# Kernel optimization log

Hardware: AMD Instinct MI355X
Metric: run time of the kernel (lower is better)

## Reference

```python
import jax, jax.numpy as jnp
import numpy as np
from math import log2

N_QUBITS = 11
N_LAYERS = 2
DEGREE = 3
N_TIMESTEPS = 8
BSZ = 64
DIM = 2 ** N_QUBITS
N_ROTS = 4 * N_QUBITS * N_LAYERS  # 88


def _ry(theta):
    # batched RY(theta): (B,) -> (B,2,2) complex64
    h = 0.5 * theta
    c, s = jnp.cos(h), jnp.sin(h)
    U = jnp.stack([jnp.stack([c, -s], -1), jnp.stack([s, c], -1)], -2)
    return U.astype(jnp.complex64)


def _rx(theta):
    # batched RX(theta): (B,) -> (B,2,2) complex64
    h = 0.5 * theta
    c = jnp.cos(h).astype(jnp.complex64)
    s = (-1j) * jnp.sin(h).astype(jnp.complex64)
    return jnp.stack([jnp.stack([c, s], -1), jnp.stack([s, c], -1)], -2)


def _apply_1q(state, U, w):
    # state: (B,) + (2,)*n ; apply per-batch 2x2 U on wire w
    s = jnp.moveaxis(state, w + 1, 1)
    shp = s.shape
    s = s.reshape(shp[0], 2, -1)
    s = jnp.einsum('bij,bjr->bir', U, s)
    return jnp.moveaxis(s.reshape(shp), 1, w + 1)


def _apply_crx(state, theta, c_w, t_w):
    # controlled-RX: apply RX on target wire t_w where control wire c_w is |1>
    U = _rx(theta)
    s = jnp.moveaxis(state, (c_w + 1, t_w + 1), (1, 2))
    shp = s.shape
    s = s.reshape(shp[0], 2, 2, -1)
    s1 = jnp.einsum('bij,bjr->bir', U, s[:, 1])
    s = jnp.concatenate([s[:, :1], s1[:, None]], axis=1).reshape(shp)
    return jnp.moveaxis(s, (1, 2), (c_w + 1, t_w + 1))


def _sim14_evolve(state, params):
    # faithful sim14_circuit (v3 fixed RY-CRX gate set), batched angles
    n = state.ndim - 1
    layers = params.shape[1] // (4 * n)
    idx = 0
    for _ in range(layers):
        for i in range(n):
            state = _apply_1q(state, _ry(params[:, idx]), i); idx += 1
        for i in range(n - 1, -1, -1):
            state = _apply_crx(state, params[:, idx], i, (i + 1) % n); idx += 1
        for i in range(n):
            state = _apply_1q(state, _ry(params[:, idx]), i); idx += 1
        for i in [n - 1] + list(range(n - 1)):
            state = _apply_crx(state, params[:, idx], i, (i - 1) % n); idx += 1
    return state


def _apply_unitaries(base, uparams, coeffs):
    # apply_unitaries_pl: repeat_interleave + evolve + LCU einsum
    bsz, T, n_rots = uparams.shape
    dim = base.shape[1]
    n = int(round(log2(dim)))
    flat = uparams.reshape(bsz * T, n_rots)
    rep = jnp.repeat(base, T, axis=0).reshape((bsz * T,) + (2,) * n)
    ev = _sim14_evolve(rep, flat).reshape(bsz, T, dim)
    return jnp.einsum('bti,bt->bi', ev, coeffs.astype(jnp.complex64))


def setup_inputs() -> dict:
    key = jax.random.key(0)
    k1, k2, k3, k4 = jax.random.split(key, 4)
    base_states = jax.random.normal(k1, (BSZ, DIM), dtype=jnp.float32)
    unitary_params = jax.random.normal(k2, (BSZ, N_TIMESTEPS, N_ROTS), dtype=jnp.float32)
    lcu_coeffs = jax.random.normal(k3, (BSZ, N_TIMESTEPS), dtype=jnp.float32)
    poly_coeffs = jax.random.normal(k4, (DEGREE + 1,), dtype=jnp.float32)
    return {"base_states": base_states, "unitary_params": unitary_params,
            "lcu_coeffs": lcu_coeffs, "poly_coeffs": poly_coeffs}


def reference(base_states, unitary_params, lcu_coeffs, poly_coeffs):
    # evaluate_polynomial_state_pl (QSVT polynomial state preparation)
    base = base_states.astype(jnp.complex64)
    base = base / jnp.linalg.norm(base, axis=1, keepdims=True)  # valid quantum state
    pc = poly_coeffs.astype(jnp.complex64)
    acc = pc[0] * base
    working = base
    for k in range(1, poly_coeffs.shape[0]):
        working = _apply_unitaries(working, unitary_params, lcu_coeffs)
        acc = acc + pc[k] * working
    out = acc / jnp.sum(jnp.abs(poly_coeffs)).astype(jnp.complex64)
    # return real/imag stacked so output is real-valued: (bsz, dim, 2)
    return jnp.stack([out.real, out.imag], axis=-1)
```

## Files before the change

kernel.cpp:

```cpp
#include <hip/hip_runtime.h>
#include <utility>

#define DIM 2048
#define NQ 11
#define NROT 88
#define BSZ 64
#define NT 8
#define NPC 4

#if __has_builtin(__builtin_amdgcn_permlane16_swap)
#define HAVE_PL16 1
#else
#define HAVE_PL16 0
#endif
#if __has_builtin(__builtin_amdgcn_permlane32_swap)
#define HAVE_PL32 1
#else
#define HAVE_PL32 0
#endif

constexpr int g_type(int G) {
    int j = G % 44;
    return (j < 11 || (j >= 22 && j < 33)) ? 0 : 1;
}
constexpr int g_pt(int G) {
    int j = G % 44;
    if (j < 11) return 10 - j;
    if (j < 22) { int i = 21 - j; int tw = (i + 1 == NQ) ? 0 : i + 1; return 10 - tw; }
    if (j < 33) return 10 - (j - 22);
    if (j == 33) return 1;
    int i = j - 34; int tw = (i + 10) % NQ; return 10 - tw;
}
constexpr int g_pcb(int G) {
    int j = G % 44;
    if (j >= 11 && j < 22) { int i = 21 - j; return 10 - i; }
    if (j == 33) return 0;
    if (j >= 34) { int i = j - 34; return 10 - i; }
    return -1;
}
constexpr int block_parity(int G) {
    int c = 0;
    for (int g = 0; g < G; ++g) if (g_pt(g) >= 8) c ^= 1;
    return c;
}
constexpr bool use_sum_tier(int lb) {
    return (lb == 4 && HAVE_PL16) || (lb == 5 && HAVE_PL32);
}

template<int G>
__device__ __forceinline__ void get_cs(float c0, float s0, float c1, float s1,
                                       float& c, float& s) {
    if constexpr (G < 64) {
        c = __int_as_float(__builtin_amdgcn_readlane(__float_as_int(c0), G));
        s = __int_as_float(__builtin_amdgcn_readlane(__float_as_int(s0), G));
    } else {
        c = __int_as_float(__builtin_amdgcn_readlane(__float_as_int(c1), G - 64));
        s = __int_as_float(__builtin_amdgcn_readlane(__float_as_int(s1), G - 64));
    }
}

template<int LB>
__device__ __forceinline__ float lxp(float x) {
    if constexpr (LB == 0) {
        return __int_as_float(__builtin_amdgcn_update_dpp(
            __float_as_int(x), __float_as_int(x), 0xB1, 0xF, 0xF, true));
    } else if constexpr (LB == 1) {
        return __int_as_float(__builtin_amdgcn_update_dpp(
            __float_as_int(x), __float_as_int(x), 0x4E, 0xF, 0xF, true));
    } else if constexpr (LB == 2) {
        return __int_as_float(__builtin_amdgcn_ds_swizzle(__float_as_int(x), 0x101F));
    } else if constexpr (LB == 3) {
        return __int_as_float(__builtin_amdgcn_update_dpp(
            __float_as_int(x), __float_as_int(x), 0x128, 0xF, 0xF, true));
    } else if constexpr (LB == 4) {
        return __int_as_float(__builtin_amdgcn_ds_swizzle(__float_as_int(x), 0x401F));
    } else {
        return __shfl_xor(x, 32, 64);
    }
}

template<int LB>
__device__ __forceinline__ float lxsum(float x) {
#if HAVE_PL16
    if constexpr (LB == 4) {
        unsigned u = __float_as_uint(x);
        auto r = __builtin_amdgcn_permlane16_swap(u, u, false, false);
        return __uint_as_float(r[0]) + __uint_as_float(r[1]);
    }
#endif
#if HAVE_PL32
    if constexpr (LB == 5) {
        unsigned u = __float_as_uint(x);
        auto r = __builtin_amdgcn_permlane32_swap(u, u, false, false);
        return __uint_as_float(r[0]) + __uint_as_float(r[1]);
    }
#endif
    return x + lxp<LB>(x);
}

template<int G>
__device__ __forceinline__ void apply_gate(
    float2 (&R)[2], float2 (&I)[2],
    float c0, float s0, float c1, float s1,
    float4* __restrict__ exbuf, const int tid)
{
    constexpr int type = g_type(G);
    constexpr int pt   = g_pt(G);
    constexpr int pcb  = g_pcb(G);
    float c, s;
    get_cs<G>(c0, s0, c1, s1, c, s);

    if constexpr (pt == 0) {
        if constexpr (type == 0) {
#pragma unroll
            for (int m = 0; m < 2; ++m) {
                float er = R[m].x, orr = R[m].y, ei = I[m].x, oi = I[m].y;
                R[m].x = c*er - s*orr;  R[m].y = s*er + c*orr;
                I[m].x = c*ei - s*oi;   I[m].y = s*ei + c*oi;
            }
        } else if constexpr (pcb == 1) {
            float er = R[1].x, orr = R[1].y, ei = I[1].x, oi = I[1].y;
            R[1].x = c*er + s*oi;   I[1].x = c*ei - s*orr;
            R[1].y = c*orr + s*ei;  I[1].y = c*oi - s*er;
        } else {
            const bool ctrl = (tid >> (pcb - 2)) & 1;
            if (ctrl) {
#pragma unroll
                for (int m = 0; m < 2; ++m) {
                    float er = R[m].x, orr = R[m].y, ei = I[m].x, oi = I[m].y;
                    R[m].x = c*er + s*oi;   I[m].x = c*ei - s*orr;
                    R[m].y = c*orr + s*ei;  I[m].y = c*oi - s*er;
                }
            }
        }
    } else if constexpr (pt == 1) {
        if constexpr (type == 0) {
            float2 l = R[0], h = R[1], li = I[0], hi = I[1];
            R[0].x = c*l.x - s*h.x;   R[0].y = c*l.y - s*h.y;
            R[1].x = s*l.x + c*h.x;   R[1].y = s*l.y + c*h.y;
            I[0].x = c*li.x - s*hi.x; I[0].y = c*li.y - s*hi.y;
            I[1].x = s*li.x + c*hi.x; I[1].y = s*li.y + c*hi.y;
        } else if constexpr (pcb == 0) {
            float lr = R[0].y, li = I[0].y, hr = R[1].y, hi = I[1].y;
            R[0].y = c*lr + s*hi;   I[0].y = c*li - s*hr;
            R[1].y = c*hr + s*li;   I[1].y = c*hi - s*lr;
        } else {
            const bool ctrl = (tid >> (pcb - 2)) & 1;
            if (ctrl) {
                float2 l = R[0], h = R[1], li = I[0], hi = I[1];
                R[0].x = c*l.x + s*hi.x;  R[0].y = c*l.y + s*hi.y;
                I[0].x = c*li.x - s*h.x;  I[0].y = c*li.y - s*h.y;
                R[1].x = c*h.x + s*li.x;  R[1].y = c*h.y + s*li.y;
                I[1].x = c*hi.x - s*l.x;  I[1].y = c*hi.y - s*l.y;
            }
        }
    } else if constexpr (pt <= 7) {
        constexpr int lb = pt - 2;
        if constexpr (use_sum_tier(lb)) {
            if constexpr (type == 0) {
                const float sg = ((tid >> lb) & 1) ? s : -s;
                const float k1 = c - sg;
#pragma unroll
                for (int m = 0; m < 2; ++m) {
                    float srx = lxsum<lb>(R[m].x), sry = lxsum<lb>(R[m].y);
                    float six = lxsum<lb>(I[m].x), siy = lxsum<lb>(I[m].y);
                    R[m].x = k1*R[m].x + sg*srx;  R[m].y = k1*R[m].y + sg*sry;
                    I[m].x = k1*I[m].x + sg*six;  I[m].y = k1*I[m].y + sg*siy;
                }
            } else if constexpr (pcb == 0) {
#pragma unroll
                for (int m = 0; m < 2; ++m) {
                    float sR = lxsum<lb>(R[m].y), sI = lxsum<lb>(I[m].y);
                    float r = R[m].y, i = I[m].y;
                    R[m].y = c*r - s*i + s*sI;
                    I[m].y = c*i + s*r - s*sR;
                }
            } else if constexpr (pcb == 1) {
                float sRx = lxsum<lb>(R[1].x), sRy = lxsum<lb>(R[1].y);
                float sIx = lxsum<lb>(I[1].x), sIy = lxsum<lb>(I[1].y);
                float rx = R[1].x, ry = R[1].y, ix = I[1].x, iy = I[1].y;
                R[1].x = c*rx - s*ix + s*sIx;  R[1].y = c*ry - s*iy + s*sIy;
                I[1].x = c*ix + s*rx - s*sRx;  I[1].y = c*iy + s*ry - s*sRy;
            } else {
                const bool ctrl = (tid >> (pcb - 2)) & 1;
                if (ctrl) {
#pragma unroll
                    for (int m = 0; m < 2; ++m) {
                        float sRx = lxsum<lb>(R[m].x), sRy = lxsum<lb>(R[m].y);
                        float sIx = lxsum<lb>(I[m].x), sIy = lxsum<lb>(I[m].y);
                        float rx = R[m].x, ry = R[m].y, ix = I[m].x, iy = I[m].y;
                        R[m].x = c*rx - s*ix + s*sIx;  R[m].y = c*ry - s*iy + s*sIy;
                        I[m].x = c*ix + s*rx - s*sRx;  I[m].y = c*iy + s*ry - s*sRy;
                    }
                }
            }
        } else {
            if constexpr (type == 0) {
                const float sg = ((tid >> lb) & 1) ? s : -s;
#pragma unroll
                for (int m = 0; m < 2; ++m) {
                    float prx = lxp<lb>(R[m].x), pry = lxp<lb>(R[m].y);
                    float pix = lxp<lb>(I[m].x), piy = lxp<lb>(I[m].y);
                    R[m].x = c*R[m].x + sg*prx;  R[m].y = c*R[m].y + sg*pry;
                    I[m].x = c*I[m].x + sg*pix;  I[m].y = c*I[m].y + sg*piy;
                }
            } else if constexpr (pcb == 0) {
#pragma unroll
                for (int m = 0; m < 2; ++m) {
                    float pry = lxp<lb>(R[m].y), piy = lxp<lb>(I[m].y);
                    R[m].y = c*R[m].y + s*piy;
                    I[m].y = c*I[m].y - s*pry;
                }
            } else if constexpr (pcb == 1) {
                float prx = lxp<lb>(R[1].x), pry = lxp<lb>(R[1].y);
                float pix = lxp<lb>(I[1].x), piy = lxp<lb>(I[1].y);
                R[1].x = c*R[1].x + s*pix;  R[1].y = c*R[1].y + s*piy;
                I[1].x = c*I[1].x - s*prx;  I[1].y = c*I[1].y - s*pry;
            } else {
                const bool ctrl = (tid >> (pcb - 2)) & 1;
                if (ctrl) {
#pragma unroll
                    for (int m = 0; m < 2; ++m) {
                        float prx = lxp<lb>(R[m].x), pry = lxp<lb>(R[m].y);
                        float pix = lxp<lb>(I[m].x), piy = lxp<lb>(I[m].y);
                        R[m].x = c*R[m].x + s*pix;  R[m].y = c*R[m].y + s*piy;
                        I[m].x = c*I[m].x - s*prx;  I[m].y = c*I[m].y - s*pry;
                    }
                }
            }
        }
    } else {
        constexpr int par = block_parity(G);
        float4* buf = exbuf + par * 1024;
        const int ptid = tid ^ (1 << (pt - 2));
        if constexpr (type == 0) {
#pragma unroll
            for (int m = 0; m < 2; ++m)
                buf[m * 512 + tid] = make_float4(R[m].x, R[m].y, I[m].x, I[m].y);
            __syncthreads();
            const float sg = ((tid >> (pt - 2)) & 1) ? s : -s;
#pragma unroll
            for (int m = 0; m < 2; ++m) {
                float4 v = buf[m * 512 + ptid];
                R[m].x = c*R[m].x + sg*v.x;  R[m].y = c*R[m].y + sg*v.y;
                I[m].x = c*I[m].x + sg*v.z;  I[m].y = c*I[m].y + sg*v.w;
            }
        } else if constexpr (pcb == 0) {
            float2* f2 = (float2*)buf;
#pragma unroll
            for (int m = 0; m < 2; ++m)
                f2[m * 512 + tid] = make_float2(R[m].y, I[m].y);
            __syncthreads();
#pragma unroll
            for (int m = 0; m < 2; ++m) {
                float2 v = f2[m * 512 + ptid];
                R[m].y = c*R[m].y + s*v.y;
                I[m].y = c*I[m].y - s*v.x;
            }
        } else if constexpr (pcb == 1) {
            buf[tid] = make_float4(R[1].x, R[1].y, I[1].x, I[1].y);
            __syncthreads();
            float4 v = buf[ptid];
            R[1].x = c*R[1].x + s*v.z;  R[1].y = c*R[1].y + s*v.w;
            I[1].x = c*I[1].x - s*v.x;  I[1].y = c*I[1].y - s*v.y;
        } else {
            const bool ctrl = (tid >> (pcb - 2)) & 1;
            if (ctrl) {
#pragma unroll
                for (int m = 0; m < 2; ++m)
                    buf[m * 512 + tid] = make_float4(R[m].x, R[m].y, I[m].x, I[m].y);
            }
            __syncthreads();
            if (ctrl) {
#pragma unroll
                for (int m = 0; m < 2; ++m) {
                    float4 v = buf[m * 512 + ptid];
                    R[m].x = c*R[m].x + s*v.z;  R[m].y = c*R[m].y + s*v.w;
                    I[m].x = c*I[m].x - s*v.x;  I[m].y = c*I[m].y - s*v.y;
                }
            }
        }
    }
}

template<int... Gs>
__device__ __forceinline__ void apply_all(std::integer_sequence<int, Gs...>,
    float2 (&R)[2], float2 (&I)[2],
    float c0, float s0, float c1, float s1,
    float4* __restrict__ exbuf, const int tid)
{
    (apply_gate<Gs>(R, I, c0, s0, c1, s1, exbuf, tid), ...);
}

template<int MODE>
__global__ __launch_bounds__(512, 4) void evolve_kernel(
    const void* __restrict__ src, const float* __restrict__ uparams,
    const float* __restrict__ lcu, float2* __restrict__ pout,
    const float* __restrict__ pcoef, float2* __restrict__ acc, int kprev)
{
    __shared__ float4 exbuf[2048];
    __shared__ float red[9];

    const int b = blockIdx.x >> 3;
    const int t = blockIdx.x & 7;
    const int tid = threadIdx.x;
    const int lane = tid & 63;

    const float* __restrict__ th_row = uparams + (size_t)(b * NT + t) * NROT;
    float th0 = 0.5f * th_row[lane];
    float th1 = (lane < NROT - 64) ? 0.5f * th_row[64 + lane] : 0.f;
    float tc0 = cosf(th0), ts0 = sinf(th0);
    float tc1 = cosf(th1), ts1 = sinf(th1);

    float2 R[2], I[2];
    if constexpr (MODE == 0) {
        const float4* b4 = (const float4*)((const float*)src + (size_t)b * DIM);
        float4 v = b4[tid];
        float loc = v.x*v.x + v.y*v.y + v.z*v.z + v.w*v.w;
        for (int off = 32; off > 0; off >>= 1) loc += __shfl_down(loc, off, 64);
        if ((tid & 63) == 0) red[tid >> 6] = loc;
        __syncthreads();
        if (tid == 0) { float sm = 0.f; for (int w = 0; w < 8; ++w) sm += red[w]; red[8] = sm; }
        __syncthreads();
        const float inv = rsqrtf(red[8]);
        R[0] = make_float2(v.x * inv, v.y * inv);
        R[1] = make_float2(v.z * inv, v.w * inv);
        I[0] = make_float2(0.f, 0.f);
        I[1] = make_float2(0.f, 0.f);
        if (t == 0) {
            const float p0 = pcoef[0];
            float4* a4 = (float4*)(acc + (size_t)b * DIM);
            a4[tid*2+0] = make_float4(p0*R[0].x, 0.f, p0*R[0].y, 0.f);
            a4[tid*2+1] = make_float4(p0*R[1].x, 0.f, p0*R[1].y, 0.f);
        }
    } else if constexpr (MODE == 1) {
        R[0] = R[1] = I[0] = I[1] = make_float2(0.f, 0.f);
        const float2* s2 = (const float2*)src;
        for (int cc = 0; cc < NT; ++cc) {
            const float4* p4 = (const float4*)(s2 + ((size_t)b * NT + cc) * DIM);
#pragma unroll
            for (int m = 0; m < 2; ++m) {
                float4 v = p4[tid*2+m];
                R[m].x += v.x; I[m].x += v.y; R[m].y += v.z; I[m].y += v.w;
            }
        }
        if (t == 0) {
            const float pk = pcoef[kprev];
            float4* a4 = (float4*)(acc + (size_t)b * DIM);
#pragma unroll
            for (int m = 0; m < 2; ++m) {
                float4 v = a4[tid*2+m];
                v.x += pk * R[m].x; v.y += pk * I[m].x;
                v.z += pk * R[m].y; v.w += pk * I[m].y;
                a4[tid*2+m] = v;
            }
        }
    } else {
        const float2* s2 = (const float2*)src;
        const float4* p4 = (const float4*)(s2 + (size_t)b * DIM);
#pragma unroll
        for (int m = 0; m < 2; ++m) {
            float4 v = p4[tid*2+m];
            R[m].x = v.x; I[m].x = v.y; R[m].y = v.z; I[m].y = v.w;
        }
    }

    apply_all(std::make_integer_sequence<int, NROT>{}, R, I,
              tc0, ts0, tc1, ts1, exbuf, tid);

    const float coeff = lcu[b * NT + t];
    float4* o4 = (float4*)(pout + ((size_t)b * NT + t) * DIM);
#pragma unroll
    for (int m = 0; m < 2; ++m)
        o4[tid*2+m] = make_float4(coeff*R[m].x, coeff*I[m].x, coeff*R[m].y, coeff*I[m].y);
}

__global__ __launch_bounds__(256) void final_kernel(
    const float2* __restrict__ partial, const float* __restrict__ pcoef,
    const float2* __restrict__ acc, float* __restrict__ out)
{
    int b = blockIdx.x >> 3;
    int i = ((blockIdx.x & 7) << 8) | threadIdx.x;
    float sr = 0.f, si = 0.f;
    for (int c = 0; c < NT; ++c) {
        float2 v = partial[((size_t)b * NT + c) * DIM + i];
        sr += v.x; si += v.y;
    }
    float sabs = 0.f;
    for (int q = 0; q < NPC; ++q) sabs += fabsf(pcoef[q]);
    float invn = 1.0f / sabs;
    float pk = pcoef[NPC - 1];
    float2 a = acc[(size_t)b * DIM + i];
    out[((size_t)b * DIM + i) * 2 + 0] = (a.x + pk * sr) * invn;
    out[((size_t)b * DIM + i) * 2 + 1] = (a.y + pk * si) * invn;
}

__global__ __launch_bounds__(256) void setup_kernel(
    const float* __restrict__ base, const float* __restrict__ pc,
    float2* __restrict__ working, float2* __restrict__ acc)
{
    int b = blockIdx.x;
    int tid = threadIdx.x;
    __shared__ float red[4];
    float ssum = 0.f;
    for (int i = tid; i < DIM; i += 256) {
        float v = base[b * DIM + i];
        ssum += v * v;
    }
    for (int off = 32; off > 0; off >>= 1) ssum += __shfl_down(ssum, off, 64);
    if ((tid & 63) == 0) red[tid >> 6] = ssum;
    __syncthreads();
    if (tid == 0) red[0] = red[0] + red[1] + red[2] + red[3];
    __syncthreads();
    float inv = rsqrtf(red[0]);
    float p0 = pc[0];
    for (int i = tid; i < DIM; i += 256) {
        float v = base[b * DIM + i] * inv;
        working[b * DIM + i] = make_float2(v, 0.f);
        acc[b * DIM + i] = make_float2(p0 * v, 0.f);
    }
}

__global__ __launch_bounds__(256) void reduce_kernel(
    const float2* __restrict__ partial, const float* __restrict__ pcoef,
    float2* __restrict__ working, float2* __restrict__ acc,
    float* __restrict__ out, int k, int last)
{
    int b = blockIdx.x >> 3;
    int i = ((blockIdx.x & 7) << 8) | threadIdx.x;
    float pk = pcoef[k];
    float sr = 0.f, si = 0.f;
    for (int c = 0; c < NT; ++c) {
        float2 v = partial[((size_t)b * NT + c) * DIM + i];
        sr += v.x; si += v.y;
    }
    working[b * DIM + i] = make_float2(sr, si);
    float2 a = acc[b * DIM + i];
    a.x += pk * sr; a.y += pk * si;
    acc[b * DIM + i] = a;
    if (last) {
        float sabs = 0.f;
        for (int q = 0; q < NPC; ++q) sabs += fabsf(pcoef[q]);
        float invn = 1.0f / sabs;
        out[((size_t)b * DIM + i) * 2 + 0] = a.x * invn;
        out[((size_t)b * DIM + i) * 2 + 1] = a.y * invn;
    }
}

extern "C" void kernel_launch(void* const* d_in, const int* in_sizes, int n_in,
                              void* d_out, int out_size, void* d_ws, size_t ws_size,
                              hipStream_t stream) {
    const float* base = (const float*)d_in[0];
    const float* upar = (const float*)d_in[1];
    const float* lcu  = (const float*)d_in[2];
    const float* pc   = (const float*)d_in[3];
    float* out = (float*)d_out;

    const size_t plane = (size_t)BSZ * DIM * sizeof(float2);
    char* ws = (char*)d_ws;

    if (ws_size >= (1 + 3 * (size_t)NT) * plane) {
        float2* acc = (float2*)ws;
        float2* pA  = (float2*)(ws + plane);
        float2* pB  = (float2*)(ws + plane + (size_t)NT * plane);
        float2* pC  = (float2*)(ws + plane + (size_t)2 * NT * plane);
        evolve_kernel<0><<<BSZ * NT, 512, 0, stream>>>(base, upar, lcu, pA, pc, acc, 0);
        evolve_kernel<1><<<BSZ * NT, 512, 0, stream>>>(pA,   upar, lcu, pB, pc, acc, 1);
        evolve_kernel<1><<<BSZ * NT, 512, 0, stream>>>(pB,   upar, lcu, pC, pc, acc, 2);
        final_kernel<<<BSZ * 8, 256, 0, stream>>>(pC, pc, acc, out);
    } else {
        float2* working = (float2*)ws;
        float2* acc     = (float2*)(ws + plane);
        float2* pA      = (float2*)(ws + 2 * plane);
        setup_kernel<<<BSZ, 256, 0, stream>>>(base, pc, working, acc);
        for (int k = 1; k <= NPC - 1; ++k) {
            evolve_kernel<2><<<BSZ * NT, 512, 0, stream>>>(working, upar, lcu, pA, pc, acc, 0);
            reduce_kernel<<<BSZ * 8, 256, 0, stream>>>(pA, pc, working, acc, out,
                                                       k, (k == NPC - 1) ? 1 : 0);
        }
    }
}
```

Before: 90.09 us.

## Replace per-gate LDS exchanges with qubit-permuting transposes between gate groups

Gates on high qubits (bits 8-10, which span thread-block positions) previously each needed their own shared-memory exchange and barrier. The gate sequence is now reordered into 96 ops, with four swizzled shared-memory transposes that swap qubit bits (2,3,5)<->(8,9,10). This lets most gates run in registers or via intra-wave lane permutes. It cuts the number of block-wide barriers and LDS round trips, at the cost of full-state transposes and more complex gate bookkeeping.

New measurement: 85.24 us. 5.4% less time.

```diff
diff --git a/kernel.cpp b/kernel.cpp
--- a/kernel.cpp
+++ b/kernel.cpp
@@ -38,14 +38,37 @@
     if (j >= 34) { int i = j - 34; return 10 - i; }
     return -1;
 }
-constexpr int block_parity(int G) {
-    int c = 0;
-    for (int g = 0; g < G; ++g) if (g_pt(g) >= 8) c ^= 1;
-    return c;
-}
 constexpr bool use_sum_tier(int lb) {
     return (lb == 4 && HAVE_PL16) || (lb == 5 && HAVE_PL32);
 }
+
+constexpr int tmap(int b) {
+    if (b == 2) return 8;  if (b == 8) return 2;
+    if (b == 3) return 9;  if (b == 9) return 3;
+    if (b == 5) return 10; if (b == 10) return 5;
+    return b;
+}
+
+constexpr int lop_j(int k) {
+    if (k < 8)  return 3 + k;
+    if (k == 8) return -1;
+    if (k < 12) return k - 9;
+    if (k == 12) return 11;
+    if (k == 13) return -1;
+    if (k < 22) return 12 + (k - 14);
+    if (k == 22) return -1;
+    if (k == 23) return 20;
+    if (k == 24) return 21;
+    if (k < 31) { int w[6] = {0, 1, 2, 3, 9, 10}; return 22 + w[k - 25]; }
+    if (k < 36) return 33 + (k - 31);
+    if (k == 36) return -1;
+    if (k < 42) return 26 + (k - 37);
+    return 38 + (k - 42);
+}
+constexpr bool lop_B(int k) {
+    return (k >= 9 && k <= 12) || (k >= 23 && k <= 35);
+}
+constexpr int lop_tpar(int k) { return (k == 8 || k == 22) ? 0 : 1; }
 
 template<int G>
 __device__ __forceinline__ void get_cs(float c0, float s0, float c1, float s1,
@@ -98,15 +121,17 @@
     return x + lxp<LB>(x);
 }
 
-template<int G>
+template<int G, bool PB>
 __device__ __forceinline__ void apply_gate(
     float2 (&R)[2], float2 (&I)[2],
     float c0, float s0, float c1, float s1,
     float4* __restrict__ exbuf, const int tid)
 {
     constexpr int type = g_type(G);
-    constexpr int pt   = g_pt(G);
-    constexpr int pcb  = g_pcb(G);
+    constexpr int pt0  = g_pt(G);
+    constexpr int pcb0 = g_pcb(G);
+    constexpr int pt   = PB ? tmap(pt0) : pt0;
+    constexpr int pcb  = (pcb0 < 0) ? -1 : (PB ? tmap(pcb0) : pcb0);
     float c, s;
     get_cs<G>(c0, s0, c1, s1, c, s);
 
@@ -229,67 +254,52 @@
                 }
             }
         }
-    } else {
-        constexpr int par = block_parity(G);
-        float4* buf = exbuf + par * 1024;
-        const int ptid = tid ^ (1 << (pt - 2));
-        if constexpr (type == 0) {
-#pragma unroll
-            for (int m = 0; m < 2; ++m)
-                buf[m * 512 + tid] = make_float4(R[m].x, R[m].y, I[m].x, I[m].y);
-            __syncthreads();
-            const float sg = ((tid >> (pt - 2)) & 1) ? s : -s;
-#pragma unroll
-            for (int m = 0; m < 2; ++m) {
-                float4 v = buf[m * 512 + ptid];
-                R[m].x = c*R[m].x + sg*v.x;  R[m].y = c*R[m].y + sg*v.y;
-                I[m].x = c*I[m].x + sg*v.z;  I[m].y = c*I[m].y + sg*v.w;
-            }
-        } else if constexpr (pcb == 0) {
-            float2* f2 = (float2*)buf;
-#pragma unroll
-            for (int m = 0; m < 2; ++m)
-                f2[m * 512 + tid] = make_float2(R[m].y, I[m].y);
-            __syncthreads();
-#pragma unroll
-            for (int m = 0; m < 2; ++m) {
-                float2 v = f2[m * 512 + ptid];
-                R[m].y = c*R[m].y + s*v.y;
-                I[m].y = c*I[m].y - s*v.x;
-            }
-        } else if constexpr (pcb == 1) {
-            buf[tid] = make_float4(R[1].x, R[1].y, I[1].x, I[1].y);
-            __syncthreads();
-            float4 v = buf[ptid];
-            R[1].x = c*R[1].x + s*v.z;  R[1].y = c*R[1].y + s*v.w;
-            I[1].x = c*I[1].x - s*v.x;  I[1].y = c*I[1].y - s*v.y;
-        } else {
-            const bool ctrl = (tid >> (pcb - 2)) & 1;
-            if (ctrl) {
-#pragma unroll
-                for (int m = 0; m < 2; ++m)
-                    buf[m * 512 + tid] = make_float4(R[m].x, R[m].y, I[m].x, I[m].y);
-            }
-            __syncthreads();
-            if (ctrl) {
-#pragma unroll
-                for (int m = 0; m < 2; ++m) {
-                    float4 v = buf[m * 512 + ptid];
-                    R[m].x = c*R[m].x + s*v.z;  R[m].y = c*R[m].y + s*v.w;
-                    I[m].x = c*I[m].x - s*v.x;  I[m].y = c*I[m].y - s*v.y;
-                }
-            }
-        }
-    }
-}
-
-template<int... Gs>
-__device__ __forceinline__ void apply_all(std::integer_sequence<int, Gs...>,
+    }
+}
+
+__device__ __forceinline__ int swz(int s) { return s ^ ((s >> 7) & 7); }
+
+template<int PAR>
+__device__ __forceinline__ void transpose_swap(float2 (&R)[2], float2 (&I)[2],
+                                               float4* __restrict__ exbuf, const int tid)
+{
+    float4* buf = exbuf + PAR * 1024;
+    const int d06 = ((tid >> 0) ^ (tid >> 6)) & 1;
+    const int d17 = ((tid >> 1) ^ (tid >> 7)) & 1;
+    const int d38 = ((tid >> 3) ^ (tid >> 8)) & 1;
+    const int q = tid ^ (d06 * 65) ^ (d17 * 130) ^ (d38 * 264);
+    buf[swz(tid * 2 + 0)] = make_float4(R[0].x, R[0].y, I[0].x, I[0].y);
+    buf[swz(tid * 2 + 1)] = make_float4(R[1].x, R[1].y, I[1].x, I[1].y);
+    __syncthreads();
+    float4 v0 = buf[swz(q * 2 + 0)];
+    float4 v1 = buf[swz(q * 2 + 1)];
+    R[0] = make_float2(v0.x, v0.y); I[0] = make_float2(v0.z, v0.w);
+    R[1] = make_float2(v1.x, v1.y); I[1] = make_float2(v1.z, v1.w);
+}
+
+template<int K>
+__device__ __forceinline__ void apply_op(
     float2 (&R)[2], float2 (&I)[2],
     float c0, float s0, float c1, float s1,
     float4* __restrict__ exbuf, const int tid)
 {
-    (apply_gate<Gs>(R, I, c0, s0, c1, s1, exbuf, tid), ...);
+    constexpr int layer = K / 48;
+    constexpr int k = K % 48;
+    constexpr int j = lop_j(k);
+    if constexpr (j < 0) {
+        transpose_swap<lop_tpar(k)>(R, I, exbuf, tid);
+    } else {
+        apply_gate<layer * 44 + j, lop_B(k)>(R, I, c0, s0, c1, s1, exbuf, tid);
+    }
+}
+
+template<int... Ks>
+__device__ __forceinline__ void apply_all(std::integer_sequence<int, Ks...>,
+    float2 (&R)[2], float2 (&I)[2],
+    float c0, float s0, float c1, float s1,
+    float4* __restrict__ exbuf, const int tid)
+{
+    (apply_op<Ks>(R, I, c0, s0, c1, s1, exbuf, tid), ...);
 }
 
 template<int MODE>
@@ -365,7 +375,7 @@
         }
     }
 
-    apply_all(std::make_integer_sequence<int, NROT>{}, R, I,
+    apply_all(std::make_integer_sequence<int, 96>{}, R, I,
               tc0, ts0, tc1, ts1, exbuf, tid);
 
     const float coeff = lcu[b * NT + t];
```
